# Kernel optimization log

Measured on AMD Instinct MI355X. Metric: run time of the kernel, lower is better.

The kernel has to match this reference:

```python
import jax, jax.numpy as jnp
import numpy as np

T, B, IN, H, L = 512, 32, 512, 512, 2  # seq_len, batch, input_size, hidden_size, num_layers
D = 2  # bidirectional
EPS = 1e-5


def setup_inputs() -> dict:
    key = jax.random.key(0)
    ks = jax.random.split(key, 4)
    s = 0.05
    return {
        "x": jax.random.normal(ks[0], (T, B, IN), jnp.float32),
        "h0": jnp.zeros((L * D, B, H), jnp.float32),
        # stacked per (layer, direction) params; index = 2*layer + dir (dir 0 = fwd, 1 = back)
        "Wx": jax.random.normal(ks[1], (L * D, IN, 3 * H), jnp.float32) * s,
        "Wh": jax.random.normal(ks[2], (L * D, H, 3 * H), jnp.float32) * s,
        "bx": jnp.zeros((L * D, 3 * H), jnp.float32),
        "bh": jnp.zeros((L * D, 3 * H), jnp.float32),
        "gx": jnp.ones((L * D, 3 * H), jnp.float32),   # LN affine scale for input proj
        "bex": jnp.zeros((L * D, 3 * H), jnp.float32), # LN affine shift for input proj
        "gh": jnp.ones((L * D, 3 * H), jnp.float32),   # LN affine scale for recurrent proj
        "beh": jnp.zeros((L * D, 3 * H), jnp.float32), # LN affine shift for recurrent proj
    }


def _ln3(a, g, b):
    # per-gate LayerNorm: a is [B, 3H]; normalize each H-sized gate chunk
    Bn, H3 = a.shape
    Hh = H3 // 3
    a = a.reshape(Bn, 3, Hh)
    mu = a.mean(-1, keepdims=True)
    var = ((a - mu) ** 2).mean(-1, keepdims=True)
    a = (a - mu) * jax.lax.rsqrt(var + EPS)
    a = a * g.reshape(3, Hh) + b.reshape(3, Hh)
    return a.reshape(Bn, H3)


def _run_dir(xs, h, Wx, Wh, bx, bh, gx, bex, gh, beh):
    # xs: [T, B, F], h: [B, H]; scan LNGRU cell over time
    def step(h, x):
        ax = _ln3(x @ Wx + bx, gx, bex)
        ah = _ln3(h @ Wh + bh, gh, beh)
        axr, axz, axn = jnp.split(ax, 3, axis=-1)
        ahr, ahz, ahn = jnp.split(ah, 3, axis=-1)
        r = jax.nn.sigmoid(axr + ahr)
        z = jax.nn.sigmoid(axz + ahz)
        n = jnp.tanh(axn + r * ahn)
        h_new = (1.0 - z) * n + z * h
        return h_new, h_new
    hT, ys = jax.lax.scan(step, h, xs)
    return hT, ys


def reference(x, h0, Wx, Wh, bx, bh, gx, bex, gh, beh):
    ff, back = x, x
    hiddens = []
    for layer in range(L):
        i = 2 * layer
        hT, ff = _run_dir(ff, h0[i], Wx[i], Wh[i], bx[i], bh[i], gx[i], bex[i], gh[i], beh[i])
        hiddens.append(hT)
        j = 2 * layer + 1
        hT, yb = _run_dir(back[::-1], h0[j], Wx[j], Wh[j], bx[j], bh[j], gx[j], bex[j], gh[j], beh[j])
        back = yb[::-1]
        hiddens.append(hT)
    output = jnp.concatenate([ff, back], axis=-1)  # [T, B, 2H]
    return output, jnp.stack(hiddens)  # hiddens: [L*2, B, H]
```

## Files before the change

kernel.cpp:

```cpp
#include <hip/hip_runtime.h>

#define T_N 512
#define B_N 32
#define H_N 512
#define G3 1536
#define NBLK 192
#define NT 1024
#define EPS_LN 1e-5f
#define OUT_HID_OFF (T_N * B_N * 1024)
#define COLL_BID 16

#define WS_STATS 448
#define WS_DOTS  (WS_STATS + 1536)
#define WS_HBUF  (WS_DOTS + 4 * B_N * G3)
#define WS_Y0    (WS_HBUF + 2 * B_N * H_N)

#define WLDS_F 32256
#define HL_F   8256
#define LDS_BYTES ((WLDS_F + HL_F + 256) * 4)

__device__ __forceinline__ float cload(const float* p) {
  return __hip_atomic_load(p, __ATOMIC_RELAXED, __HIP_MEMORY_SCOPE_AGENT);
}
__device__ __forceinline__ void cstore(float* p, float v) {
  __hip_atomic_store(p, v, __ATOMIC_RELAXED, __HIP_MEMORY_SCOPE_AGENT);
}
union U64F2 { unsigned long long u; float f[2]; };
__device__ __forceinline__ U64F2 cload2(const float* p) {
  U64F2 r;
  r.u = __hip_atomic_load((const unsigned long long*)p, __ATOMIC_RELAXED,
                          __HIP_MEMORY_SCOPE_AGENT);
  return r;
}

__device__ __forceinline__ void gbar(unsigned* barbase, unsigned& epoch, int bid) {
  epoch++;
  unsigned* arr = barbase;
  unsigned* rel = barbase + 256;
  __builtin_amdgcn_s_waitcnt(0);
  __syncthreads();
  const int tid = threadIdx.x;
  if (tid == 0)
    __hip_atomic_store(&arr[bid], epoch, __ATOMIC_RELAXED, __HIP_MEMORY_SCOPE_AGENT);
  if (bid == COLL_BID) {
    if (tid < NBLK) {
      while (__hip_atomic_load(&arr[tid], __ATOMIC_RELAXED, __HIP_MEMORY_SCOPE_AGENT) < epoch)
        __builtin_amdgcn_s_sleep(1);
    }
    __syncthreads();
    if (tid == 0)
      __hip_atomic_store(rel, epoch, __ATOMIC_RELAXED, __HIP_MEMORY_SCOPE_AGENT);
  } else {
    if (tid == 0) {
      while (__hip_atomic_load(rel, __ATOMIC_RELAXED, __HIP_MEMORY_SCOPE_AGENT) < epoch)
        __builtin_amdgcn_s_sleep(1);
    }
  }
  __syncthreads();
}

#define FMA16(WA, WB, R1, R2) do { \
  acc[0][0][0]=fmaf((R1).x,(WA).x,acc[0][0][0]); acc[0][0][1]=fmaf((R1).y,(WA).y,acc[0][0][1]); \
  acc[0][0][2]=fmaf((R1).z,(WA).z,acc[0][0][2]); acc[0][0][3]=fmaf((R1).w,(WA).w,acc[0][0][3]); \
  acc[0][1][0]=fmaf((R2).x,(WA).x,acc[0][1][0]); acc[0][1][1]=fmaf((R2).y,(WA).y,acc[0][1][1]); \
  acc[0][1][2]=fmaf((R2).z,(WA).z,acc[0][1][2]); acc[0][1][3]=fmaf((R2).w,(WA).w,acc[0][1][3]); \
  acc[1][0][0]=fmaf((R1).x,(WB).x,acc[1][0][0]); acc[1][0][1]=fmaf((R1).y,(WB).y,acc[1][0][1]); \
  acc[1][0][2]=fmaf((R1).z,(WB).z,acc[1][0][2]); acc[1][0][3]=fmaf((R1).w,(WB).w,acc[1][0][3]); \
  acc[1][1][0]=fmaf((R2).x,(WB).x,acc[1][1][0]); acc[1][1][1]=fmaf((R2).y,(WB).y,acc[1][1][1]); \
  acc[1][1][2]=fmaf((R2).z,(WB).z,acc[1][1][2]); acc[1][1][3]=fmaf((R2).w,(WB).w,acc[1][1][3]); \
} while (0)

__global__ void __launch_bounds__(NT, 1)
lngru13(const float* __restrict__ x, const float* __restrict__ h0,
        const float* __restrict__ Wx, const float* __restrict__ Wh,
        const float* __restrict__ bx, const float* __restrict__ bh,
        const float* __restrict__ gx, const float* __restrict__ bex,
        const float* __restrict__ gh, const float* __restrict__ beh,
        float* __restrict__ out, float* __restrict__ ws)
{
  extern __shared__ __align__(16) float smem[];
  float* wlds = smem;
  float* hl   = smem + WLDS_F;
  float* sred = smem + WLDS_F + HL_F;

  unsigned* barbase = (unsigned*)ws;
  float* stats = ws + WS_STATS;
  float* dots  = ws + WS_DOTS;
  float* hbuf  = ws + WS_HBUF;
  float* y0    = ws + WS_Y0;

  const int tid  = threadIdx.x;
  const int lane = tid & 63;
  const int wv   = tid >> 6;
  const int bid  = blockIdx.x;
  const int bs   = bid & 1;
  const int jt   = (bid >> 1) % 24;
  const int kd   = (bid >> 1) / 24;
  const int kind = kd & 1;
  const int d    = kd >> 1;
  const int j0   = jt * 64;
  const int g    = jt >> 3;
  const int b0   = bs * 16;
  const bool is_gate = (kind == 0) && (jt < 8);

  const bool gw  = (wv < 4);
  const int jq   = wv & 3;
  const int jj   = lane & 7;
  const int boct = lane >> 3;
  const int jla  = jq * 8 + jj;
  const int jlb  = jla + 32;

  unsigned epoch = 0;

  for (int ph = 0; ph < 2; ++ph) {
    const int widx = ph * 2 + d;

    const float* wgl = (kind ? Wh : Wx) + (size_t)widx * H_N * G3 + j0;
    for (int kk = 0; kk < 32; ++kk) {
      int k = wv * 32 + kk;
      if (k < 504)
        wlds[(k >> 2) * 256 + lane * 4 + (k & 3)] = wgl[(size_t)k * G3 + lane];
    }
    float4 wt[2][2];
    if (gw) {
#pragma unroll
      for (int h = 0; h < 2; ++h) {
        wt[0][h].x = wgl[(size_t)(504 + 4*h + 0) * G3 + jla];
        wt[0][h].y = wgl[(size_t)(504 + 4*h + 1) * G3 + jla];
        wt[0][h].z = wgl[(size_t)(504 + 4*h + 2) * G3 + jla];
        wt[0][h].w = wgl[(size_t)(504 + 4*h + 3) * G3 + jla];
        wt[1][h].x = wgl[(size_t)(504 + 4*h + 0) * G3 + jlb];
        wt[1][h].y = wgl[(size_t)(504 + 4*h + 1) * G3 + jlb];
        wt[1][h].z = wgl[(size_t)(504 + 4*h + 2) * G3 + jlb];
        wt[1][h].w = wgl[(size_t)(504 + 4*h + 3) * G3 + jlb];
      }
    }

    if (is_gate) {
      cstore(&hbuf[(d * B_N + b0 + wv) * H_N + j0 + lane],
             h0[(widx * B_N + b0 + wv) * H_N + j0 + lane]);
    }
    gbar(barbase, epoch, bid);

    const float  bva  = (kind ? bh : bx)[widx * G3 + j0 + jla];
    const float  bvb  = (kind ? bh : bx)[widx * G3 + j0 + jlb];
    const float* xsrc = (ph == 0) ? x : (y0 + (size_t)d * T_N * B_N * H_N);
    const float* hsrc = hbuf + (d * B_N + b0) * H_N;
    const float4* wqa = (const float4*)wlds + jla;
    const float4* wqb = (const float4*)wlds + jlb;
    const float*  h1  = hl + boct * 516;
    const float*  h2  = hl + (boct + 8) * 516;

    for (int s = 0; s < T_N; ++s) {
      const int t = d ? (T_N - 1 - s) : s;
      const int p = s & 1;
      float* stp = stats + p * 768;

      if (kind) {
#pragma unroll
        for (int q = 0; q < 4; ++q) {
          int e = (tid + q * 1024) * 2;
          U64F2 v = cload2(hsrc + e);
          int bb = e >> 9, k = e & 511;
          hl[bb * 516 + k]     = v.f[0];
          hl[bb * 516 + k + 1] = v.f[1];
        }
        __syncthreads();
      }

      float acc[2][2][4] = {{{0.f,0.f,0.f,0.f},{0.f,0.f,0.f,0.f}},
                            {{0.f,0.f,0.f,0.f},{0.f,0.f,0.f,0.f}}};
      if (gw) {
        if (kind) {
#pragma unroll 3
          for (int k4 = 0; k4 < 126; ++k4) {
            float4 wa = wqa[k4 * 64];
            float4 wb = wqb[k4 * 64];
            float4 r1 = *(const float4*)(h1 + k4 * 4);
            float4 r2 = *(const float4*)(h2 + k4 * 4);
            FMA16(wa, wb, r1, r2);
          }
          {
            float4 r1a = *(const float4*)(h1 + 504);
            float4 r1b = *(const float4*)(h1 + 508);
            float4 r2a = *(const float4*)(h2 + 504);
            float4 r2b = *(const float4*)(h2 + 508);
            FMA16(wt[0][0], wt[1][0], r1a, r2a);
            FMA16(wt[0][1], wt[1][1], r1b, r2b);
          }
        } else {
          const float* rp1 = xsrc + ((size_t)t * B_N + b0 + boct) * H_N;
          const float* rp2 = rp1 + 8 * H_N;
#pragma unroll 6
          for (int k4 = 0; k4 < 126; ++k4) {
            float4 wa = wqa[k4 * 64];
            float4 wb = wqb[k4 * 64];
            float4 r1 = *(const float4*)(rp1 + k4 * 4);
            float4 r2 = *(const float4*)(rp2 + k4 * 4);
            FMA16(wa, wb, r1, r2);
          }
          {
            float4 r1a = *(const float4*)(rp1 + 504);
            float4 r1b = *(const float4*)(rp1 + 508);
            float4 r2a = *(const float4*)(rp2 + 504);
            float4 r2b = *(const float4*)(rp2 + 508);
            FMA16(wt[0][0], wt[1][0], r1a, r2a);
            FMA16(wt[0][1], wt[1][1], r1b, r2b);
          }
        }
      }

      if (gw) {
        float ta1 = bva + (acc[0][0][0] + acc[0][0][1]) + (acc[0][0][2] + acc[0][0][3]);
        float ta2 = bva + (acc[0][1][0] + acc[0][1][1]) + (acc[0][1][2] + acc[0][1][3]);
        float tb1 = bvb + (acc[1][0][0] + acc[1][0][1]) + (acc[1][0][2] + acc[1][0][3]);
        float tb2 = bvb + (acc[1][1][0] + acc[1][1][1]) + (acc[1][1][2] + acc[1][1][3]);

        float* dr1 = &dots[(size_t)(kd * B_N + b0 + boct) * G3 + j0];
        float* dr2 = dr1 + (size_t)8 * G3;
        cstore(dr1 + jla, ta1);
        cstore(dr1 + jlb, tb1);
        cstore(dr2 + jla, ta2);
        cstore(dr2 + jlb, tb2);

        float s1a = ta1 + tb1, s2a = ta1 * ta1 + tb1 * tb1;
        float s1b = ta2 + tb2, s2b = ta2 * ta2 + tb2 * tb2;
        s1a += __shfl_xor(s1a, 1, 64); s2a += __shfl_xor(s2a, 1, 64);
        s1b += __shfl_xor(s1b, 1, 64); s2b += __shfl_xor(s2b, 1, 64);
        s1a += __shfl_xor(s1a, 2, 64); s2a += __shfl_xor(s2a, 2, 64);
        s1b += __shfl_xor(s1b, 2, 64); s2b += __shfl_xor(s2b, 2, 64);
        s1a += __shfl_xor(s1a, 4, 64); s2a += __shfl_xor(s2a, 4, 64);
        s1b += __shfl_xor(s1b, 4, 64); s2b += __shfl_xor(s2b, 4, 64);
        if (jj == 0) {
          sred[(boct * 4 + jq) * 2 + 0] = s1a;
          sred[(boct * 4 + jq) * 2 + 1] = s2a;
          sred[((boct + 8) * 4 + jq) * 2 + 0] = s1b;
          sred[((boct + 8) * 4 + jq) * 2 + 1] = s2b;
        }
      }
      __syncthreads();
      if (tid < 32) {
        int bl = tid >> 1, st = tid & 1;
        float a2 = 0.f;
#pragma unroll
        for (int q = 0; q < 4; ++q) a2 += sred[(bl * 4 + q) * 2 + st];
        atomicAdd(&stp[((kd * 3 + g) * B_N + b0 + bl) * 2 + st], a2);
      }

      gbar(barbase, epoch, bid);

      if (bid == NBLK - 1) {
        float* so = stats + (p ^ 1) * 768;
        if (tid < 768) cstore(so + tid, 0.f);
      }
      if (is_gate) {
        const int c  = j0 + lane;
        const int gb = b0 + wv;
        float a[2][3];
#pragma unroll
        for (int k2 = 0; k2 < 2; ++k2) {
          const float* dr  = dots + ((d * 2 + k2) * B_N + gb) * G3;
          const float* gam = (k2 ? gh : gx) + widx * G3;
          const float* bet = (k2 ? beh : bex) + widx * G3;
#pragma unroll
          for (int g2 = 0; g2 < 3; ++g2) {
            float v = cload(dr + g2 * H_N + c);
            const float* sl = stp + (((d * 2 + k2) * 3 + g2) * B_N + gb) * 2;
            float mu  = cload(sl)     * (1.f / 512.f);
            float var = cload(sl + 1) * (1.f / 512.f) - mu * mu;
            float inv = rsqrtf(var + EPS_LN);
            int J = g2 * H_N + c;
            a[k2][g2] = (v - mu) * inv * gam[J] + bet[J];
          }
        }
        float r = 1.f / (1.f + __expf(-(a[0][0] + a[1][0])));
        float z = 1.f / (1.f + __expf(-(a[0][1] + a[1][1])));
        float n = tanhf(a[0][2] + r * a[1][2]);
        float* hp = hbuf + (d * B_N + gb) * H_N + c;
        float hnew = (1.f - z) * n + z * cload(hp);
        cstore(hp, hnew);
        if (ph == 0) {
          cstore(&y0[(((size_t)d * T_N + t) * B_N + gb) * H_N + c], hnew);
        } else {
          out[((size_t)t * B_N + gb) * 1024 + d * H_N + c] = hnew;
        }
        if (s == T_N - 1) {
          out[OUT_HID_OFF + (widx * B_N + gb) * H_N + c] = hnew;
        }
      }
      gbar(barbase, epoch, bid);
    }
  }
}

extern "C" void kernel_launch(void* const* d_in, const int* in_sizes, int n_in,
                              void* d_out, int out_size, void* d_ws, size_t ws_size,
                              hipStream_t stream) {
  const float* x    = (const float*)d_in[0];
  const float* h0   = (const float*)d_in[1];
  const float* Wx   = (const float*)d_in[2];
  const float* Wh   = (const float*)d_in[3];
  const float* bxp  = (const float*)d_in[4];
  const float* bhp  = (const float*)d_in[5];
  const float* gxp  = (const float*)d_in[6];
  const float* bexp = (const float*)d_in[7];
  const float* ghp  = (const float*)d_in[8];
  const float* behp = (const float*)d_in[9];
  float* out = (float*)d_out;
  float* ws  = (float*)d_ws;

  hipMemsetAsync(d_ws, 0, 8192, stream);

  hipFuncSetAttribute((const void*)lngru13,
                      hipFuncAttributeMaxDynamicSharedMemorySize, LDS_BYTES);

  void* args[] = {(void*)&x, (void*)&h0, (void*)&Wx, (void*)&Wh, (void*)&bxp, (void*)&bhp,
                  (void*)&gxp, (void*)&bexp, (void*)&ghp, (void*)&behp, (void*)&out, (void*)&ws};
  hipLaunchCooperativeKernel((void*)lngru13, dim3(NBLK), dim3(NT), args, LDS_BYTES, stream);
}
```

Before: 21.39 ms.

## Halve grid barriers per step: redundant gate compute in recurrent blocks, x-projection one step ahead

Each recurrent (Wh) block now recomputes the full gate update for its batch half and keeps h in LDS, so h no longer makes a global round trip and the second grid barrier per step goes away. The input projection runs one step ahead, writing to triple-buffered dot slots and quad-buffered stats, so it overlaps the recurrent step. The cost is redundant elementwise gate work across the 24 recurrent blocks per direction and more workspace buffers. Correctness depends on the buffer rotation and zeroing of stats slots being right.

```diff
diff --git a/kernel.cpp b/kernel.cpp
--- a/kernel.cpp
+++ b/kernel.cpp
@@ -11,9 +11,11 @@
 #define COLL_BID 16
 
 #define WS_STATS 448
-#define WS_DOTS  (WS_STATS + 1536)
-#define WS_HBUF  (WS_DOTS + 4 * B_N * G3)
-#define WS_Y0    (WS_HBUF + 2 * B_N * H_N)
+#define STSLOT   768
+#define WS_AXD   (WS_STATS + 4 * STSLOT)
+#define DSLOT    (2 * B_N * G3)
+#define WS_AHD   (WS_AXD + 3 * DSLOT)
+#define WS_Y0    (WS_AHD + 2 * DSLOT)
 
 #define WLDS_F 32256
 #define HL_F   8256
@@ -24,13 +26,6 @@
 }
 __device__ __forceinline__ void cstore(float* p, float v) {
   __hip_atomic_store(p, v, __ATOMIC_RELAXED, __HIP_MEMORY_SCOPE_AGENT);
-}
-union U64F2 { unsigned long long u; float f[2]; };
-__device__ __forceinline__ U64F2 cload2(const float* p) {
-  U64F2 r;
-  r.u = __hip_atomic_load((const unsigned long long*)p, __ATOMIC_RELAXED,
-                          __HIP_MEMORY_SCOPE_AGENT);
-  return r;
 }
 
 __device__ __forceinline__ void gbar(unsigned* barbase, unsigned& epoch, int bid) {
@@ -71,7 +66,7 @@
 } while (0)
 
 __global__ void __launch_bounds__(NT, 1)
-lngru13(const float* __restrict__ x, const float* __restrict__ h0,
+lngru14(const float* __restrict__ x, const float* __restrict__ h0,
         const float* __restrict__ Wx, const float* __restrict__ Wh,
         const float* __restrict__ bx, const float* __restrict__ bh,
         const float* __restrict__ gx, const float* __restrict__ bex,
@@ -85,8 +80,8 @@
 
   unsigned* barbase = (unsigned*)ws;
   float* stats = ws + WS_STATS;
-  float* dots  = ws + WS_DOTS;
-  float* hbuf  = ws + WS_HBUF;
+  float* axd   = ws + WS_AXD;
+  float* ahd   = ws + WS_AHD;
   float* y0    = ws + WS_Y0;
 
   const int tid  = threadIdx.x;
@@ -101,7 +96,7 @@
   const int j0   = jt * 64;
   const int g    = jt >> 3;
   const int b0   = bs * 16;
-  const bool is_gate = (kind == 0) && (jt < 8);
+  const bool writer = (kind == 1) && (jt == 0);
 
   const bool gw  = (wv < 4);
   const int jq   = wv & 3;
@@ -115,6 +110,8 @@
   for (int ph = 0; ph < 2; ++ph) {
     const int widx = ph * 2 + d;
 
+    gbar(barbase, epoch, bid);
+
     const float* wgl = (kind ? Wh : Wx) + (size_t)widx * H_N * G3 + j0;
     for (int kk = 0; kk < 32; ++kk) {
       int k = wv * 32 + kk;
@@ -122,7 +119,10 @@
         wlds[(k >> 2) * 256 + lane * 4 + (k & 3)] = wgl[(size_t)k * G3 + lane];
     }
     float4 wt[2][2];
+    float  bva = 0.f, bvb = 0.f;
     if (gw) {
+      bva = (kind ? bh : bx)[widx * G3 + j0 + jla];
+      bvb = (kind ? bh : bx)[widx * G3 + j0 + jlb];
 #pragma unroll
       for (int h = 0; h < 2; ++h) {
         wt[0][h].x = wgl[(size_t)(504 + 4*h + 0) * G3 + jla];
@@ -135,39 +135,21 @@
         wt[1][h].w = wgl[(size_t)(504 + 4*h + 3) * G3 + jlb];
       }
     }
-
-    if (is_gate) {
-      cstore(&hbuf[(d * B_N + b0 + wv) * H_N + j0 + lane],
-             h0[(widx * B_N + b0 + wv) * H_N + j0 + lane]);
-    }
-    gbar(barbase, epoch, bid);
-
-    const float  bva  = (kind ? bh : bx)[widx * G3 + j0 + jla];
-    const float  bvb  = (kind ? bh : bx)[widx * G3 + j0 + jlb];
+    if (kind) {
+#pragma unroll
+      for (int q = 0; q < 8; ++q)
+        hl[wv * 516 + lane + 64*q] =
+            h0[((size_t)widx * B_N + b0 + wv) * H_N + lane + 64*q];
+    }
+    __syncthreads();
+
     const float* xsrc = (ph == 0) ? x : (y0 + (size_t)d * T_N * B_N * H_N);
-    const float* hsrc = hbuf + (d * B_N + b0) * H_N;
     const float4* wqa = (const float4*)wlds + jla;
     const float4* wqb = (const float4*)wlds + jlb;
     const float*  h1  = hl + boct * 516;
     const float*  h2  = hl + (boct + 8) * 516;
 
-    for (int s = 0; s < T_N; ++s) {
-      const int t = d ? (T_N - 1 - s) : s;
-      const int p = s & 1;
-      float* stp = stats + p * 768;
-
-      if (kind) {
-#pragma unroll
-        for (int q = 0; q < 4; ++q) {
-          int e = (tid + q * 1024) * 2;
-          U64F2 v = cload2(hsrc + e);
-          int bb = e >> 9, k = e & 511;
-          hl[bb * 516 + k]     = v.f[0];
-          hl[bb * 516 + k + 1] = v.f[1];
-        }
-        __syncthreads();
-      }
-
+    auto run_step = [&](int ss) {
       float acc[2][2][4] = {{{0.f,0.f,0.f,0.f},{0.f,0.f,0.f,0.f}},
                             {{0.f,0.f,0.f,0.f},{0.f,0.f,0.f,0.f}}};
       if (gw) {
@@ -189,6 +171,7 @@
             FMA16(wt[0][1], wt[1][1], r1b, r2b);
           }
         } else {
+          const int t = d ? (T_N - 1 - ss) : ss;
           const float* rp1 = xsrc + ((size_t)t * B_N + b0 + boct) * H_N;
           const float* rp2 = rp1 + 8 * H_N;
 #pragma unroll 6
@@ -209,14 +192,15 @@
           }
         }
       }
-
+      float* dd  = kind ? (ahd + (ss & 1) * DSLOT) : (axd + (ss % 3) * DSLOT);
+      float* stp = stats + (ss & 3) * STSLOT;
       if (gw) {
         float ta1 = bva + (acc[0][0][0] + acc[0][0][1]) + (acc[0][0][2] + acc[0][0][3]);
         float ta2 = bva + (acc[0][1][0] + acc[0][1][1]) + (acc[0][1][2] + acc[0][1][3]);
         float tb1 = bvb + (acc[1][0][0] + acc[1][0][1]) + (acc[1][0][2] + acc[1][0][3]);
         float tb2 = bvb + (acc[1][1][0] + acc[1][1][1]) + (acc[1][1][2] + acc[1][1][3]);
 
-        float* dr1 = &dots[(size_t)(kd * B_N + b0 + boct) * G3 + j0];
+        float* dr1 = dd + (size_t)(d * B_N + b0 + boct) * G3 + j0;
         float* dr2 = dr1 + (size_t)8 * G3;
         cstore(dr1 + jla, ta1);
         cstore(dr1 + jlb, tb1);
@@ -246,49 +230,75 @@
         for (int q = 0; q < 4; ++q) a2 += sred[(bl * 4 + q) * 2 + st];
         atomicAdd(&stp[((kd * 3 + g) * B_N + b0 + bl) * 2 + st], a2);
       }
+    };
+
+    if (!kind) run_step(0);
+    gbar(barbase, epoch, bid);
+
+    for (int s = 0; s < T_N; ++s) {
+      if (kind) run_step(s);
+      else if (s < T_N - 1) run_step(s + 1);
+
+      if (bid == NBLK - 1) {
+        float* so = stats + ((s + 2) & 3) * STSLOT;
+        if (tid < 768) cstore(so + tid, 0.f);
+      }
 
       gbar(barbase, epoch, bid);
 
-      if (bid == NBLK - 1) {
-        float* so = stats + (p ^ 1) * 768;
-        if (tid < 768) cstore(so + tid, 0.f);
-      }
-      if (is_gate) {
-        const int c  = j0 + lane;
+      if (kind) {
+        const int t  = d ? (T_N - 1 - s) : s;
         const int gb = b0 + wv;
-        float a[2][3];
-#pragma unroll
-        for (int k2 = 0; k2 < 2; ++k2) {
-          const float* dr  = dots + ((d * 2 + k2) * B_N + gb) * G3;
-          const float* gam = (k2 ? gh : gx) + widx * G3;
-          const float* bet = (k2 ? beh : bex) + widx * G3;
+        const float* axr = axd + (s % 3) * DSLOT + (size_t)(d * B_N + gb) * G3;
+        const float* ahr = ahd + (s & 1) * DSLOT + (size_t)(d * B_N + gb) * G3;
+        const float* stp = stats + (s & 3) * STSLOT;
+        float mu[2][3], inv[2][3];
+#pragma unroll
+        for (int k2 = 0; k2 < 2; ++k2)
 #pragma unroll
           for (int g2 = 0; g2 < 3; ++g2) {
-            float v = cload(dr + g2 * H_N + c);
             const float* sl = stp + (((d * 2 + k2) * 3 + g2) * B_N + gb) * 2;
-            float mu  = cload(sl)     * (1.f / 512.f);
-            float var = cload(sl + 1) * (1.f / 512.f) - mu * mu;
-            float inv = rsqrtf(var + EPS_LN);
-            int J = g2 * H_N + c;
-            a[k2][g2] = (v - mu) * inv * gam[J] + bet[J];
+            float m1 = cload(sl)     * (1.f / 512.f);
+            float m2 = cload(sl + 1) * (1.f / 512.f);
+            mu[k2][g2]  = m1;
+            inv[k2][g2] = rsqrtf(m2 - m1 * m1 + EPS_LN);
+          }
+        const float* gxr = gx  + widx * G3;
+        const float* bxr = bex + widx * G3;
+        const float* ghr = gh  + widx * G3;
+        const float* bhr = beh + widx * G3;
+#pragma unroll 2
+        for (int q = 0; q < 8; ++q) {
+          const int c = lane + 64 * q;
+          float ax0 = cload(axr + c);
+          float ax1 = cload(axr + H_N + c);
+          float ax2 = cload(axr + 2 * H_N + c);
+          float ah0 = cload(ahr + c);
+          float ah1 = cload(ahr + H_N + c);
+          float ah2 = cload(ahr + 2 * H_N + c);
+          float a00 = (ax0 - mu[0][0]) * inv[0][0] * gxr[c]         + bxr[c];
+          float a01 = (ax1 - mu[0][1]) * inv[0][1] * gxr[H_N + c]   + bxr[H_N + c];
+          float a02 = (ax2 - mu[0][2]) * inv[0][2] * gxr[2*H_N + c] + bxr[2*H_N + c];
+          float a10 = (ah0 - mu[1][0]) * inv[1][0] * ghr[c]         + bhr[c];
+          float a11 = (ah1 - mu[1][1]) * inv[1][1] * ghr[H_N + c]   + bhr[H_N + c];
+          float a12 = (ah2 - mu[1][2]) * inv[1][2] * ghr[2*H_N + c] + bhr[2*H_N + c];
+          float r = 1.f / (1.f + __expf(-(a00 + a10)));
+          float z = 1.f / (1.f + __expf(-(a01 + a11)));
+          float n = tanhf(a02 + r * a12);
+          float* hp = hl + wv * 516 + c;
+          float hnew = (1.f - z) * n + z * *hp;
+          *hp = hnew;
+          if (writer) {
+            if (ph == 0)
+              cstore(&y0[(((size_t)d * T_N + t) * B_N + gb) * H_N + c], hnew);
+            else
+              out[((size_t)t * B_N + gb) * 1024 + d * H_N + c] = hnew;
+            if (s == T_N - 1)
+              out[OUT_HID_OFF + ((size_t)widx * B_N + gb) * H_N + c] = hnew;
           }
         }
-        float r = 1.f / (1.f + __expf(-(a[0][0] + a[1][0])));
-        float z = 1.f / (1.f + __expf(-(a[0][1] + a[1][1])));
-        float n = tanhf(a[0][2] + r * a[1][2]);
-        float* hp = hbuf + (d * B_N + gb) * H_N + c;
-        float hnew = (1.f - z) * n + z * cload(hp);
-        cstore(hp, hnew);
-        if (ph == 0) {
-          cstore(&y0[(((size_t)d * T_N + t) * B_N + gb) * H_N + c], hnew);
-        } else {
-          out[((size_t)t * B_N + gb) * 1024 + d * H_N + c] = hnew;
-        }
-        if (s == T_N - 1) {
-          out[OUT_HID_OFF + (widx * B_N + gb) * H_N + c] = hnew;
-        }
-      }
-      gbar(barbase, epoch, bid);
+        __syncthreads();
+      }
     }
   }
 }
@@ -309,12 +319,12 @@
   float* out = (float*)d_out;
   float* ws  = (float*)d_ws;
 
-  hipMemsetAsync(d_ws, 0, 8192, stream);
-
-  hipFuncSetAttribute((const void*)lngru13,
+  hipMemsetAsync(d_ws, 0, 16384, stream);
+
+  hipFuncSetAttribute((const void*)lngru14,
                       hipFuncAttributeMaxDynamicSharedMemorySize, LDS_BYTES);
 
   void* args[] = {(void*)&x, (void*)&h0, (void*)&Wx, (void*)&Wh, (void*)&bxp, (void*)&bhp,
                   (void*)&gxp, (void*)&bexp, (void*)&ghp, (void*)&behp, (void*)&out, (void*)&ws};
-  hipLaunchCooperativeKernel((void*)lngru13, dim3(NBLK), dim3(NT), args, LDS_BYTES, stream);
-}
+  hipLaunchCooperativeKernel((void*)lngru14, dim3(NBLK), dim3(NT), args, LDS_BYTES, stream);
+}
```

Result: no change. 21.75 ms (+1.7%).

## Split batch into two pipelined halves with dedicated barrier-coordinator block

Applied to the files above, without the earlier changes.

Halves the grid to 96 compute blocks plus one coordinator block. Each compute block now runs the projection GEMM for both batch halves in turn, and the per-step grid barrier is replaced by four phase-specific barriers. Gate updates for one half can then overlap with GEMM work on the other half, and staging of the recurrent state is split across the halves. Stats use four rotating slots. The cost is that each block does twice the GEMM work, and the extra barrier stages add latency on the critical path.

```diff
diff --git a/kernel.cpp b/kernel.cpp
--- a/kernel.cpp
+++ b/kernel.cpp
@@ -4,14 +4,23 @@
 #define B_N 32
 #define H_N 512
 #define G3 1536
-#define NBLK 192
+#define NCMP 96
+#define NBLK 97
 #define NT 1024
 #define EPS_LN 1e-5f
 #define OUT_HID_OFF (T_N * B_N * 1024)
-#define COLL_BID 16
-
-#define WS_STATS 448
-#define WS_DOTS  (WS_STATS + 1536)
+#define ZBID 16
+
+#define ARR_B10 0
+#define ARR_B11 128
+#define ARR_B20 256
+#define ARR_B21 384
+#define ARR_PH  512
+#define REL0    640
+
+#define WS_STATS 832
+#define STSLOT   768
+#define WS_DOTS  (WS_STATS + 4 * STSLOT)
 #define WS_HBUF  (WS_DOTS + 4 * B_N * G3)
 #define WS_Y0    (WS_HBUF + 2 * B_N * H_N)
 
@@ -33,28 +42,16 @@
   return r;
 }
 
-__device__ __forceinline__ void gbar(unsigned* barbase, unsigned& epoch, int bid) {
-  epoch++;
-  unsigned* arr = barbase;
-  unsigned* rel = barbase + 256;
+__device__ __forceinline__ void barr_arrive(unsigned* arr, int idx, unsigned e) {
   __builtin_amdgcn_s_waitcnt(0);
   __syncthreads();
-  const int tid = threadIdx.x;
-  if (tid == 0)
-    __hip_atomic_store(&arr[bid], epoch, __ATOMIC_RELAXED, __HIP_MEMORY_SCOPE_AGENT);
-  if (bid == COLL_BID) {
-    if (tid < NBLK) {
-      while (__hip_atomic_load(&arr[tid], __ATOMIC_RELAXED, __HIP_MEMORY_SCOPE_AGENT) < epoch)
-        __builtin_amdgcn_s_sleep(1);
-    }
-    __syncthreads();
-    if (tid == 0)
-      __hip_atomic_store(rel, epoch, __ATOMIC_RELAXED, __HIP_MEMORY_SCOPE_AGENT);
-  } else {
-    if (tid == 0) {
-      while (__hip_atomic_load(rel, __ATOMIC_RELAXED, __HIP_MEMORY_SCOPE_AGENT) < epoch)
-        __builtin_amdgcn_s_sleep(1);
-    }
+  if (threadIdx.x == 0)
+    __hip_atomic_store(arr + idx, e, __ATOMIC_RELAXED, __HIP_MEMORY_SCOPE_AGENT);
+}
+__device__ __forceinline__ void barr_wait(unsigned* rel, unsigned e) {
+  if (threadIdx.x == 0) {
+    while (__hip_atomic_load(rel, __ATOMIC_RELAXED, __HIP_MEMORY_SCOPE_AGENT) < e)
+      __builtin_amdgcn_s_sleep(1);
   }
   __syncthreads();
 }
@@ -71,7 +68,7 @@
 } while (0)
 
 __global__ void __launch_bounds__(NT, 1)
-lngru13(const float* __restrict__ x, const float* __restrict__ h0,
+lngru15(const float* __restrict__ x, const float* __restrict__ h0,
         const float* __restrict__ Wx, const float* __restrict__ Wh,
         const float* __restrict__ bx, const float* __restrict__ bh,
         const float* __restrict__ gx, const float* __restrict__ bex,
@@ -83,25 +80,64 @@
   float* hl   = smem + WLDS_F;
   float* sred = smem + WLDS_F + HL_F;
 
-  unsigned* barbase = (unsigned*)ws;
+  unsigned* bu   = (unsigned*)ws;
+  unsigned* rel  = bu + REL0;
   float* stats = ws + WS_STATS;
   float* dots  = ws + WS_DOTS;
   float* hbuf  = ws + WS_HBUF;
   float* y0    = ws + WS_Y0;
 
   const int tid  = threadIdx.x;
+  const int bid  = blockIdx.x;
+
+  if (bid == NCMP) {
+    unsigned e = 0;
+    for (int ph = 0; ph < 2; ++ph) {
+      unsigned pe = ph + 1u;
+      if (tid < NCMP)
+        while (__hip_atomic_load(bu + ARR_PH + tid, __ATOMIC_RELAXED, __HIP_MEMORY_SCOPE_AGENT) < pe)
+          __builtin_amdgcn_s_sleep(1);
+      __syncthreads();
+      if (tid == 0) __hip_atomic_store(rel + 4*32, pe, __ATOMIC_RELAXED, __HIP_MEMORY_SCOPE_AGENT);
+      for (int s = 0; s < T_N; ++s) {
+        e++;
+        if (tid < NCMP)
+          while (__hip_atomic_load(bu + ARR_B10 + tid, __ATOMIC_RELAXED, __HIP_MEMORY_SCOPE_AGENT) < e)
+            __builtin_amdgcn_s_sleep(1);
+        __syncthreads();
+        if (tid == 0) __hip_atomic_store(rel + 0*32, e, __ATOMIC_RELAXED, __HIP_MEMORY_SCOPE_AGENT);
+        if (tid < NCMP)
+          while (__hip_atomic_load(bu + ARR_B11 + tid, __ATOMIC_RELAXED, __HIP_MEMORY_SCOPE_AGENT) < e)
+            __builtin_amdgcn_s_sleep(1);
+        __syncthreads();
+        if (tid == 0) __hip_atomic_store(rel + 1*32, e, __ATOMIC_RELAXED, __HIP_MEMORY_SCOPE_AGENT);
+        if (tid < 16)
+          while (__hip_atomic_load(bu + ARR_B20 + tid, __ATOMIC_RELAXED, __HIP_MEMORY_SCOPE_AGENT) < e)
+            __builtin_amdgcn_s_sleep(1);
+        __syncthreads();
+        if (tid == 0) __hip_atomic_store(rel + 2*32, e, __ATOMIC_RELAXED, __HIP_MEMORY_SCOPE_AGENT);
+        if (tid < 16)
+          while (__hip_atomic_load(bu + ARR_B21 + tid, __ATOMIC_RELAXED, __HIP_MEMORY_SCOPE_AGENT) < e)
+            __builtin_amdgcn_s_sleep(1);
+        __syncthreads();
+        if (tid == 0) __hip_atomic_store(rel + 3*32, e, __ATOMIC_RELAXED, __HIP_MEMORY_SCOPE_AGENT);
+      }
+    }
+    return;
+  }
+
   const int lane = tid & 63;
   const int wv   = tid >> 6;
-  const int bid  = blockIdx.x;
-  const int bs   = bid & 1;
-  const int jt   = (bid >> 1) % 24;
-  const int kd   = (bid >> 1) / 24;
+  const int jt   = bid % 24;
+  const int kd   = bid / 24;
   const int kind = kd & 1;
   const int d    = kd >> 1;
   const int j0   = jt * 64;
   const int g    = jt >> 3;
-  const int b0   = bs * 16;
-  const bool is_gate = (kind == 0) && (jt < 8);
+  const bool gates0 = (kind == 0) && (jt < 8);
+  const bool gates1 = (kind == 0) && (jt >= 8) && (jt < 16);
+  const int ct   = gates0 ? jt : (jt - 8);
+  const int gidx = d * 8 + ct;
 
   const bool gw  = (wv < 4);
   const int jq   = wv & 3;
@@ -110,10 +146,9 @@
   const int jla  = jq * 8 + jj;
   const int jlb  = jla + 32;
 
-  unsigned epoch = 0;
-
   for (int ph = 0; ph < 2; ++ph) {
     const int widx = ph * 2 + d;
+    const unsigned pe = ph + 1u;
 
     const float* wgl = (kind ? Wh : Wx) + (size_t)widx * H_N * G3 + j0;
     for (int kk = 0; kk < 32; ++kk) {
@@ -122,7 +157,10 @@
         wlds[(k >> 2) * 256 + lane * 4 + (k & 3)] = wgl[(size_t)k * G3 + lane];
     }
     float4 wt[2][2];
+    float  bva = 0.f, bvb = 0.f;
     if (gw) {
+      bva = (kind ? bh : bx)[widx * G3 + j0 + jla];
+      bvb = (kind ? bh : bx)[widx * G3 + j0 + jlb];
 #pragma unroll
       for (int h = 0; h < 2; ++h) {
         wt[0][h].x = wgl[(size_t)(504 + 4*h + 0) * G3 + jla];
@@ -135,39 +173,33 @@
         wt[1][h].w = wgl[(size_t)(504 + 4*h + 3) * G3 + jlb];
       }
     }
-
-    if (is_gate) {
-      cstore(&hbuf[(d * B_N + b0 + wv) * H_N + j0 + lane],
-             h0[(widx * B_N + b0 + wv) * H_N + j0 + lane]);
-    }
-    gbar(barbase, epoch, bid);
-
-    const float  bva  = (kind ? bh : bx)[widx * G3 + j0 + jla];
-    const float  bvb  = (kind ? bh : bx)[widx * G3 + j0 + jlb];
+    if (kind) {
+#pragma unroll
+      for (int q4 = 0; q4 < 8; ++q4)
+        hl[wv * 516 + lane + 64*q4] =
+            h0[((size_t)widx * B_N + wv) * H_N + lane + 64*q4];
+    }
+    if (gates0) {
+      cstore(&hbuf[(d * B_N + wv) * H_N + ct*64 + lane],
+             h0[((size_t)widx * B_N + wv) * H_N + ct*64 + lane]);
+    }
+    if (gates1) {
+      cstore(&hbuf[(d * B_N + 16 + wv) * H_N + ct*64 + lane],
+             h0[((size_t)widx * B_N + 16 + wv) * H_N + ct*64 + lane]);
+    }
+    if (ph == 1 && bid == ZBID) {
+      for (int i = tid; i < 4 * STSLOT; i += NT) cstore(stats + i, 0.f);
+    }
+    barr_arrive(bu + ARR_PH, bid, pe);
+    barr_wait(rel + 4*32, pe);
+
     const float* xsrc = (ph == 0) ? x : (y0 + (size_t)d * T_N * B_N * H_N);
-    const float* hsrc = hbuf + (d * B_N + b0) * H_N;
     const float4* wqa = (const float4*)wlds + jla;
     const float4* wqb = (const float4*)wlds + jlb;
     const float*  h1  = hl + boct * 516;
     const float*  h2  = hl + (boct + 8) * 516;
 
-    for (int s = 0; s < T_N; ++s) {
-      const int t = d ? (T_N - 1 - s) : s;
-      const int p = s & 1;
-      float* stp = stats + p * 768;
-
-      if (kind) {
-#pragma unroll
-        for (int q = 0; q < 4; ++q) {
-          int e = (tid + q * 1024) * 2;
-          U64F2 v = cload2(hsrc + e);
-          int bb = e >> 9, k = e & 511;
-          hl[bb * 516 + k]     = v.f[0];
-          hl[bb * 516 + k + 1] = v.f[1];
-        }
-        __syncthreads();
-      }
-
+    auto run_gemm = [&](int q, int ss) {
       float acc[2][2][4] = {{{0.f,0.f,0.f,0.f},{0.f,0.f,0.f,0.f}},
                             {{0.f,0.f,0.f,0.f},{0.f,0.f,0.f,0.f}}};
       if (gw) {
@@ -180,16 +212,15 @@
             float4 r2 = *(const float4*)(h2 + k4 * 4);
             FMA16(wa, wb, r1, r2);
           }
-          {
-            float4 r1a = *(const float4*)(h1 + 504);
-            float4 r1b = *(const float4*)(h1 + 508);
-            float4 r2a = *(const float4*)(h2 + 504);
-            float4 r2b = *(const float4*)(h2 + 508);
-            FMA16(wt[0][0], wt[1][0], r1a, r2a);
-            FMA16(wt[0][1], wt[1][1], r1b, r2b);
-          }
+          float4 r1a = *(const float4*)(h1 + 504);
+          float4 r1b = *(const float4*)(h1 + 508);
+          float4 r2a = *(const float4*)(h2 + 504);
+          float4 r2b = *(const float4*)(h2 + 508);
+          FMA16(wt[0][0], wt[1][0], r1a, r2a);
+          FMA16(wt[0][1], wt[1][1], r1b, r2b);
         } else {
-          const float* rp1 = xsrc + ((size_t)t * B_N + b0 + boct) * H_N;
+          const int t = d ? (T_N - 1 - ss) : ss;
+          const float* rp1 = xsrc + ((size_t)t * B_N + q*16 + boct) * H_N;
           const float* rp2 = rp1 + 8 * H_N;
 #pragma unroll 6
           for (int k4 = 0; k4 < 126; ++k4) {
@@ -199,24 +230,19 @@
             float4 r2 = *(const float4*)(rp2 + k4 * 4);
             FMA16(wa, wb, r1, r2);
           }
-          {
-            float4 r1a = *(const float4*)(rp1 + 504);
-            float4 r1b = *(const float4*)(rp1 + 508);
-            float4 r2a = *(const float4*)(rp2 + 504);
-            float4 r2b = *(const float4*)(rp2 + 508);
-            FMA16(wt[0][0], wt[1][0], r1a, r2a);
-            FMA16(wt[0][1], wt[1][1], r1b, r2b);
-          }
+          float4 r1a = *(const float4*)(rp1 + 504);
+          float4 r1b = *(const float4*)(rp1 + 508);
+          float4 r2a = *(const float4*)(rp2 + 504);
+          float4 r2b = *(const float4*)(rp2 + 508);
+          FMA16(wt[0][0], wt[1][0], r1a, r2a);
+          FMA16(wt[0][1], wt[1][1], r1b, r2b);
         }
-      }
-
-      if (gw) {
         float ta1 = bva + (acc[0][0][0] + acc[0][0][1]) + (acc[0][0][2] + acc[0][0][3]);
         float ta2 = bva + (acc[0][1][0] + acc[0][1][1]) + (acc[0][1][2] + acc[0][1][3]);
         float tb1 = bvb + (acc[1][0][0] + acc[1][0][1]) + (acc[1][0][2] + acc[1][0][3]);
         float tb2 = bvb + (acc[1][1][0] + acc[1][1][1]) + (acc[1][1][2] + acc[1][1][3]);
 
-        float* dr1 = &dots[(size_t)(kd * B_N + b0 + boct) * G3 + j0];
+        float* dr1 = dots + (size_t)(kd * B_N + q*16 + boct) * G3 + j0;
         float* dr2 = dr1 + (size_t)8 * G3;
         cstore(dr1 + jla, ta1);
         cstore(dr1 + jlb, tb1);
@@ -243,52 +269,89 @@
         int bl = tid >> 1, st = tid & 1;
         float a2 = 0.f;
 #pragma unroll
-        for (int q = 0; q < 4; ++q) a2 += sred[(bl * 4 + q) * 2 + st];
-        atomicAdd(&stp[((kd * 3 + g) * B_N + b0 + bl) * 2 + st], a2);
-      }
-
-      gbar(barbase, epoch, bid);
-
-      if (bid == NBLK - 1) {
-        float* so = stats + (p ^ 1) * 768;
-        if (tid < 768) cstore(so + tid, 0.f);
-      }
-      if (is_gate) {
-        const int c  = j0 + lane;
-        const int gb = b0 + wv;
-        float a[2][3];
-#pragma unroll
-        for (int k2 = 0; k2 < 2; ++k2) {
-          const float* dr  = dots + ((d * 2 + k2) * B_N + gb) * G3;
-          const float* gam = (k2 ? gh : gx) + widx * G3;
-          const float* bet = (k2 ? beh : bex) + widx * G3;
-#pragma unroll
-          for (int g2 = 0; g2 < 3; ++g2) {
-            float v = cload(dr + g2 * H_N + c);
-            const float* sl = stp + (((d * 2 + k2) * 3 + g2) * B_N + gb) * 2;
-            float mu  = cload(sl)     * (1.f / 512.f);
-            float var = cload(sl + 1) * (1.f / 512.f) - mu * mu;
-            float inv = rsqrtf(var + EPS_LN);
-            int J = g2 * H_N + c;
-            a[k2][g2] = (v - mu) * inv * gam[J] + bet[J];
-          }
+        for (int qq = 0; qq < 4; ++qq) a2 += sred[(bl * 4 + qq) * 2 + st];
+        atomicAdd(&stats[(size_t)(ss & 3) * STSLOT +
+                         ((kd * 3 + g) * B_N + q*16 + bl) * 2 + st], a2);
+      }
+    };
+
+    auto run_gates = [&](int q, int ss) {
+      const int t  = d ? (T_N - 1 - ss) : ss;
+      const int gb = q*16 + wv;
+      const int c  = ct * 64 + lane;
+      const float* stp = stats + (size_t)(ss & 3) * STSLOT;
+      float a[2][3];
+#pragma unroll
+      for (int k2 = 0; k2 < 2; ++k2) {
+        const float* dr  = dots + (size_t)((d * 2 + k2) * B_N + gb) * G3;
+        const float* gam = (k2 ? gh : gx) + widx * G3;
+        const float* bet = (k2 ? beh : bex) + widx * G3;
+#pragma unroll
+        for (int g2 = 0; g2 < 3; ++g2) {
+          float v = cload(dr + g2 * H_N + c);
+          const float* sl = stp + (((d * 2 + k2) * 3 + g2) * B_N + gb) * 2;
+          float mu  = cload(sl)     * (1.f / 512.f);
+          float var = cload(sl + 1) * (1.f / 512.f) - mu * mu;
+          float inv = rsqrtf(var + EPS_LN);
+          int J = g2 * H_N + c;
+          a[k2][g2] = (v - mu) * inv * gam[J] + bet[J];
         }
-        float r = 1.f / (1.f + __expf(-(a[0][0] + a[1][0])));
-        float z = 1.f / (1.f + __expf(-(a[0][1] + a[1][1])));
-        float n = tanhf(a[0][2] + r * a[1][2]);
-        float* hp = hbuf + (d * B_N + gb) * H_N + c;
-        float hnew = (1.f - z) * n + z * cload(hp);
-        cstore(hp, hnew);
-        if (ph == 0) {
-          cstore(&y0[(((size_t)d * T_N + t) * B_N + gb) * H_N + c], hnew);
-        } else {
-          out[((size_t)t * B_N + gb) * 1024 + d * H_N + c] = hnew;
-        }
-        if (s == T_N - 1) {
-          out[OUT_HID_OFF + (widx * B_N + gb) * H_N + c] = hnew;
-        }
-      }
-      gbar(barbase, epoch, bid);
+      }
+      float r = 1.f / (1.f + __expf(-(a[0][0] + a[1][0])));
+      float z = 1.f / (1.f + __expf(-(a[0][1] + a[1][1])));
+      float n = tanhf(a[0][2] + r * a[1][2]);
+      float* hp = hbuf + (size_t)(d * B_N + gb) * H_N + c;
+      float hnew = (1.f - z) * n + z * cload(hp);
+      cstore(hp, hnew);
+      if (ph == 0)
+        cstore(&y0[(((size_t)d * T_N + t) * B_N + gb) * H_N + c], hnew);
+      else
+        out[((size_t)t * B_N + gb) * 1024 + d * H_N + c] = hnew;
+      if (ss == T_N - 1)
+        out[OUT_HID_OFF + ((size_t)widx * B_N + gb) * H_N + c] = hnew;
+    };
+
+    auto stage_h = [&](int q) {
+      const float* hsrc = hbuf + (size_t)(d * B_N + q*16) * H_N;
+#pragma unroll
+      for (int q4 = 0; q4 < 4; ++q4) {
+        int e2 = (tid + q4 * 1024) * 2;
+        U64F2 v = cload2(hsrc + e2);
+        int bb = e2 >> 9, k = e2 & 511;
+        hl[bb * 516 + k]     = v.f[0];
+        hl[bb * 516 + k + 1] = v.f[1];
+      }
+      __syncthreads();
+    };
+
+    for (int s = 0; s < T_N; ++s) {
+      const unsigned e = (unsigned)(ph * T_N + s + 1);
+
+      run_gemm(0, s);
+      barr_arrive(bu + ARR_B10, bid, e);
+
+      if (kind) stage_h(1);
+      else if (bid == ZBID) {
+        if (tid < STSLOT) cstore(stats + (size_t)((s + 2) & 3) * STSLOT + tid, 0.f);
+      }
+
+      run_gemm(1, s);
+      barr_arrive(bu + ARR_B11, bid, e);
+
+      if (gates0) {
+        barr_wait(rel + 0*32, e);
+        run_gates(0, s);
+        barr_arrive(bu + ARR_B20, gidx, e);
+      }
+      if (gates1) {
+        barr_wait(rel + 1*32, e);
+        run_gates(1, s);
+        barr_arrive(bu + ARR_B21, gidx, e);
+      }
+
+      barr_wait(rel + 2*32, e);
+      if (kind) stage_h(0);
+      barr_wait(rel + 3*32, e);
     }
   }
 }
@@ -309,12 +372,12 @@
   float* out = (float*)d_out;
   float* ws  = (float*)d_ws;
 
-  hipMemsetAsync(d_ws, 0, 8192, stream);
-
-  hipFuncSetAttribute((const void*)lngru13,
+  hipMemsetAsync(d_ws, 0, 16384, stream);
+
+  hipFuncSetAttribute((const void*)lngru15,
                       hipFuncAttributeMaxDynamicSharedMemorySize, LDS_BYTES);
 
   void* args[] = {(void*)&x, (void*)&h0, (void*)&Wx, (void*)&Wh, (void*)&bxp, (void*)&bhp,
                   (void*)&gxp, (void*)&bexp, (void*)&ghp, (void*)&behp, (void*)&out, (void*)&ws};
-  hipLaunchCooperativeKernel((void*)lngru13, dim3(NBLK), dim3(NT), args, LDS_BYTES, stream);
-}
+  hipLaunchCooperativeKernel((void*)lngru15, dim3(NBLK), dim3(NT), args, LDS_BYTES, stream);
+}
```

New measurement: 39.55 ms. 1.85x slower.
